# Performance work log

Hardware: AMD Instinct MI355X
Metric: run time of the kernel (lower is better)

Reference implementation:

```python
import jax, jax.numpy as jnp
import numpy as np

D_MODEL = 1024
NUM_HEADS = 16
D_K = D_MODEL // NUM_HEADS
THETA = 10000.0


def _rope(x, cos, sin):
    # x: [b, h, l, d_k]; cos/sin: [l, d_k//2]
    x1 = x[..., ::2]
    x2 = x[..., 1::2]
    re = x1 * cos - x2 * sin
    ro = x1 * sin + x2 * cos
    return jnp.stack([re, ro], axis=-1).reshape(x.shape)


def setup_inputs() -> dict:
    key = jax.random.key(0)
    k0, k1, k2, k3, k4 = jax.random.split(key, 5)
    b, l = 2, 2048
    scale = 1.0 / np.sqrt(D_MODEL)
    return {
        "in_features": jax.random.normal(k0, (b, l, D_MODEL), dtype=jnp.float32),
        "wq": jax.random.normal(k1, (D_MODEL, D_MODEL), dtype=jnp.float32) * scale,
        "wk": jax.random.normal(k2, (D_MODEL, D_MODEL), dtype=jnp.float32) * scale,
        "wv": jax.random.normal(k3, (D_MODEL, D_MODEL), dtype=jnp.float32) * scale,
        "wo": jax.random.normal(k4, (D_MODEL, D_MODEL), dtype=jnp.float32) * scale,
    }


def reference(in_features, wq, wk, wv, wo):
    b, l, d = in_features.shape
    h, dk = NUM_HEADS, D_K

    def proj(w):
        # torch: einsum('b l d, k d -> b l k') == x @ w.T
        y = jnp.einsum('bld,kd->blk', in_features, w)
        return y.reshape(b, l, h, dk).transpose(0, 2, 1, 3)  # [b,h,l,dk]

    Q, K, V = proj(wq), proj(wk), proj(wv)

    # RoPE (use_rope=True)
    inv_freq = 1.0 / (THETA ** (jnp.arange(0, dk, 2, dtype=jnp.float32) / dk))
    angles = jnp.arange(l, dtype=jnp.float32)[:, None] * inv_freq[None, :]  # [l, dk//2]
    cos, sin = jnp.cos(angles), jnp.sin(angles)
    Q = _rope(Q, cos, sin)
    K = _rope(K, cos, sin)

    scores = jnp.einsum('bhqd,bhkd->bhqk', Q, K) / jnp.sqrt(jnp.float32(dk))
    causal = jnp.tril(jnp.ones((l, l), dtype=bool))  # [l,l]
    scores = jnp.where(causal[None, None], scores, jnp.float32(-jnp.inf))
    attn = jax.nn.softmax(scores, axis=-1)
    ctx = jnp.einsum('bhqk,bhkd->bhqd', attn, V)
    ctx = ctx.transpose(0, 2, 1, 3).reshape(b, l, d)  # [b,l,d_model]
    out = jnp.einsum('bld,md->blm', ctx, wo)
    return out
```

## Files before the change

kernel.cpp:

```cpp
#include <hip/hip_runtime.h>
#include <stdint.h>

typedef __attribute__((ext_vector_type(8))) short short8;
typedef __attribute__((ext_vector_type(4))) float floatx4;
typedef __attribute__((ext_vector_type(16))) float floatx16;

#define DEV static __device__ __forceinline__

DEV unsigned short f2bf(float f) {
  union { float f; uint32_t u; } v; v.f = f;
  return (unsigned short)((v.u + 0x7FFFu + ((v.u >> 16) & 1u)) >> 16);
}
DEV float bf2f(unsigned short h) {
  union { uint32_t u; float f; } v; v.u = ((uint32_t)h) << 16;
  return v.f;
}
DEV uint32_t cvtpk(float lo, float hi) {
  uint32_t d;
  asm("v_cvt_pk_bf16_f32 %0, %1, %2" : "=v"(d) : "v"(lo), "v"(hi));
  return d;
}
DEV void gload_lds16(const void* g, void* l) {
  __builtin_amdgcn_global_load_lds(
      (const __attribute__((address_space(1))) uint32_t*)g,
      (__attribute__((address_space(3))) uint32_t*)l, 16, 0, 0);
}

#if defined(__has_builtin)
#if __has_builtin(__builtin_amdgcn_permlane32_swap)
#define HAVE_PLSWAP 1
#endif
#endif
DEV void plswap(uint32_t& a, uint32_t& b) {
#ifdef HAVE_PLSWAP
  typedef unsigned int u2v __attribute__((ext_vector_type(2)));
  u2v r = __builtin_amdgcn_permlane32_swap(a, b, false, false);
  a = r.x; b = r.y;
#else
  uint32_t sa = (uint32_t)__shfl_xor((int)a, 32);
  uint32_t sb = (uint32_t)__shfl_xor((int)b, 32);
  uint32_t lane = __lane_id();
  uint32_t na = lane < 32 ? a : sb;
  uint32_t nb = lane < 32 ? sa : b;
  a = na; b = nb;
#endif
}
DEV float xmax32(float x) {
  union { float f; uint32_t u; } a, b; a.f = x; b.f = x;
  plswap(a.u, b.u);
  return fmaxf(a.f, b.f);
}
DEV float xsum32(float x) {
  union { float f; uint32_t u; } a, b; a.f = x; b.f = x;
  plswap(a.u, b.u);
  return a.f + b.f;
}

__global__ __launch_bounds__(256) void k_convert(
    const float* __restrict__ X, const float* __restrict__ Wq,
    const float* __restrict__ Wk, const float* __restrict__ Wv,
    const float* __restrict__ Wo, unsigned short* __restrict__ out) {
  long gid = (long)blockIdx.x * 256 + threadIdx.x;
  long e = gid * 8;
  int seg = (int)(e >> 20);
  const float* src; long base;
  if (seg < 4)      { src = X;  base = 0; }
  else if (seg == 4){ src = Wq; base = 4l << 20; }
  else if (seg == 5){ src = Wk; base = 5l << 20; }
  else if (seg == 6){ src = Wv; base = 6l << 20; }
  else              { src = Wo; base = 7l << 20; }
  const float4* s4 = (const float4*)(src + (e - base));
  float4 a = s4[0], b = s4[1];
  union { uint4 q; unsigned short s[8]; } u;
  u.s[0] = f2bf(a.x); u.s[1] = f2bf(a.y); u.s[2] = f2bf(a.z); u.s[3] = f2bf(a.w);
  u.s[4] = f2bf(b.x); u.s[5] = f2bf(b.y); u.s[6] = f2bf(b.z); u.s[7] = f2bf(b.w);
  *(uint4*)(out + e) = u.q;
}

template <int MODE>
__global__ __launch_bounds__(256) void k_gemm(
    const unsigned short* __restrict__ A,
    const unsigned short* __restrict__ B0, const unsigned short* __restrict__ B1,
    const unsigned short* __restrict__ B2,
    unsigned short* __restrict__ Qo, unsigned short* __restrict__ Ko,
    unsigned short* __restrict__ VFo, float* __restrict__ Cf, int K) {
  __shared__ unsigned short At[128 * 64];
  __shared__ unsigned short Bt[128 * 64];
  const int tid = threadIdx.x, lane = tid & 63, wid = tid >> 6;
  const int wm = (wid >> 1) * 64, wn = (wid & 1) * 64;
  const int g = lane >> 4, c0 = lane & 15;
  const int bm0 = blockIdx.x * 128;
  const int bnG = blockIdx.y * 128;
  const unsigned short* Bp;
  int bn0;
  if constexpr (MODE == 0) {
    int wsel = bnG >> 10;
    Bp = wsel == 0 ? B0 : (wsel == 1 ? B1 : B2);
    bn0 = bnG & 1023;
  } else { Bp = B0; bn0 = bnG; }
  floatx4 acc[4][4] = {};
  const int nk = K >> 6;
  const int koff = (blockIdx.x + blockIdx.y * 3) & (nk - 1);
  const int swzr = (c0 & 7) << 4;
  for (int s = 0; s < nk; ++s) {
    const int kt = ((s + koff) & (nk - 1)) << 6;
#pragma unroll
    for (int i = 0; i < 4; ++i) {
      int o = (wid * 64 + lane) * 16 + i * 4096;
      int row = o >> 7;
      int col = (o & 127) ^ ((row & 7) << 4);
      int k0 = col >> 1;
      gload_lds16((const char*)A  + ((long)(bm0 + row) * K + kt + k0) * 2, (char*)At + o);
      gload_lds16((const char*)Bp + ((long)(bn0 + row) * K + kt + k0) * 2, (char*)Bt + o);
    }
    __syncthreads();
#pragma unroll
    for (int kk = 0; kk < 2; ++kk) {
      const int kb = kk * 64 + g * 16;
      short8 av[4], bv[4];
#pragma unroll
      for (int mi = 0; mi < 4; ++mi)
        av[mi] = *(const short8*)((const char*)At + (wm + mi * 16 + c0) * 128 + (kb ^ swzr));
#pragma unroll
      for (int ni = 0; ni < 4; ++ni)
        bv[ni] = *(const short8*)((const char*)Bt + (wn + ni * 16 + c0) * 128 + (kb ^ swzr));
#pragma unroll
      for (int mi = 0; mi < 4; ++mi)
#pragma unroll
        for (int ni = 0; ni < 4; ++ni)
          acc[mi][ni] = __builtin_amdgcn_mfma_f32_16x16x32_bf16(av[mi], bv[ni], acc[mi][ni], 0, 0, 0);
    }
    __syncthreads();
  }
  if constexpr (MODE == 1) {
#pragma unroll
    for (int mi = 0; mi < 4; ++mi)
#pragma unroll
      for (int ni = 0; ni < 4; ++ni)
#pragma unroll
        for (int i = 0; i < 4; ++i) {
          int r = bm0 + wm + mi * 16 + 4 * g + i;
          int cg = bnG + wn + ni * 16 + c0;
          Cf[(long)r * 1024 + cg] = acc[mi][ni][i];
        }
  } else {
    const int wsel = bnG >> 10;
#pragma unroll
    for (int mi = 0; mi < 4; ++mi)
#pragma unroll
      for (int ni = 0; ni < 4; ++ni)
#pragma unroll
        for (int i = 0; i < 4; ++i) {
          int r = bm0 + wm + mi * 16 + 4 * g + i;
          int cg = bnG + wn + ni * 16 + c0;
          int cc = cg & 1023, head = cc >> 6, dkk = cc & 63;
          int bb = r >> 11, ll = r & 2047;
          long bh = bb * 16 + head;
          float v = acc[mi][ni][i];
          if (wsel == 2) {
            int T = ll >> 6, rt = ll & 63;
            int m = rt >> 4, hb = (rt >> 3) & 1, j = rt & 7;
            int dvs = dkk >> 5, c = dkk & 31;
            VFo[bh * 131072 + T * 4096 + (dvs * 4 + m) * 512 + (hb * 32 + c) * 8 + j] = f2bf(v);
          } else {
            unsigned short* dst = wsel == 0 ? Qo : Ko;
            dst[(bh * 2048 + ll) * 64 + dkk] = f2bf(v);
          }
        }
  }
}

__global__ __launch_bounds__(256) void k_rope(unsigned short* __restrict__ Qd, float qscale) {
  int gid = blockIdx.x * 256 + threadIdx.x;
  int row = gid >> 1, hf = gid & 1;
  int l = row & 2047;
  unsigned short* p = Qd + (long)row * 64 + hf * 32;
  union { uint4 q[4]; unsigned short s[32]; } u;
#pragma unroll
  for (int i = 0; i < 4; ++i) u.q[i] = ((const uint4*)p)[i];
  float lf = (float)l;
#pragma unroll
  for (int j = 0; j < 16; ++j) {
    int pp = hf * 16 + j;
    float ang = lf * exp2f(-(float)pp * 0.4152410118609203f);
    float sv, cv; sincosf(ang, &sv, &cv);
    float x1 = bf2f(u.s[2 * j]), x2 = bf2f(u.s[2 * j + 1]);
    u.s[2 * j]     = f2bf((x1 * cv - x2 * sv) * qscale);
    u.s[2 * j + 1] = f2bf((x1 * sv + x2 * cv) * qscale);
  }
#pragma unroll
  for (int i = 0; i < 4; ++i) ((uint4*)p)[i] = u.q[i];
}

__global__ __launch_bounds__(256) void k_ropeK_repack(
    const unsigned short* __restrict__ Kin, unsigned short* __restrict__ KF) {
  const int blk = blockIdx.x;
  const int bh = blk >> 5, T = blk & 31;
  const int tid = threadIdx.x;
  const unsigned short* src = Kin + ((long)bh * 2048 + T * 64) * 64;
  unsigned short* dst = KF + (long)blk * 4096;
#pragma unroll
  for (int it = 0; it < 2; ++it) {
    int u = tid + it * 256;
    int lane = u & 63, kd = u >> 6;
    int kvs = kd >> 2, dseg = kd & 3;
    int row = kvs * 32 + (lane & 31);
    int col = dseg * 16 + 8 * (lane >> 5);
    union { uint4 q; unsigned short s[8]; } v;
    v.q = *(const uint4*)(src + row * 64 + col);
    float lf = (float)(T * 64 + row);
#pragma unroll
    for (int j = 0; j < 4; ++j) {
      int p = (col >> 1) + j;
      float ang = lf * exp2f(-(float)p * 0.4152410118609203f);
      float sv, cv; sincosf(ang, &sv, &cv);
      float x1 = bf2f(v.s[2 * j]), x2 = bf2f(v.s[2 * j + 1]);
      v.s[2 * j]     = f2bf(x1 * cv - x2 * sv);
      v.s[2 * j + 1] = f2bf(x1 * sv + x2 * cv);
    }
    *(uint4*)(dst + u * 8) = v.q;
  }
}

DEV void attn_tile(int T, int Tend, int ntm1, int qabs, int h, int c,
                   const unsigned short* __restrict__ kfbase,
                   const unsigned short* __restrict__ vfbase,
                   const short8 (&qf)[4],
                   const short8 (&kc0)[4], const short8 (&kc1)[4],
                   short8 (&kn0)[4], short8 (&kn1)[4],
                   floatx16& ctx0, floatx16& ctx1, float& m_, float& l_) {
  {
    const int Tn = T + 1 < Tend ? T + 1 : T;
    const unsigned short* kt = kfbase + (long)Tn * 4096;
#pragma unroll
    for (int d = 0; d < 4; ++d) kn0[d] = *(const short8*)(kt + d * 512);
#pragma unroll
    for (int d = 0; d < 4; ++d) kn1[d] = *(const short8*)(kt + 2048 + d * 512);
  }
  const unsigned short* vt = vfbase + (long)T * 4096;
  short8 vf0[4], vf1[4];
#pragma unroll
  for (int m = 0; m < 4; ++m) vf0[m] = *(const short8*)(vt + m * 512);
#pragma unroll
  for (int m = 0; m < 4; ++m) vf1[m] = *(const short8*)(vt + 2048 + m * 512);

  floatx16 s0 = {}, s1 = {};
#pragma unroll
  for (int d = 0; d < 4; ++d)
    s0 = __builtin_amdgcn_mfma_f32_32x32x16_bf16(kc0[d], qf[d], s0, 0, 0, 0);
#pragma unroll
  for (int d = 0; d < 4; ++d)
    s1 = __builtin_amdgcn_mfma_f32_32x32x16_bf16(kc1[d], qf[d], s1, 0, 0, 0);

  if (T == ntm1) {
    const int kvb = T * 64 + 4 * h;
#pragma unroll
    for (int r = 0; r < 16; ++r) {
      const int off = (r & 3) + 8 * (r >> 2);
      if (kvb + off > qabs) s0[r] = -1e30f;
      if (kvb + 32 + off > qabs) s1[r] = -1e30f;
    }
  }
  float a4[8];
#pragma unroll
  for (int j = 0; j < 4; ++j) {
    a4[j]     = fmaxf(fmaxf(s0[4 * j], s0[4 * j + 1]), fmaxf(s0[4 * j + 2], s0[4 * j + 3]));
    a4[4 + j] = fmaxf(fmaxf(s1[4 * j], s1[4 * j + 1]), fmaxf(s1[4 * j + 2], s1[4 * j + 3]));
  }
  float mx = fmaxf(fmaxf(fmaxf(a4[0], a4[1]), fmaxf(a4[2], a4[3])),
                   fmaxf(fmaxf(a4[4], a4[5]), fmaxf(a4[6], a4[7])));
  mx = xmax32(mx);
  if (!__all(mx <= m_ + 8.0f)) {
    float mn = fmaxf(m_, mx);
    float sc = exp2f(m_ - mn);
    m_ = mn;
    l_ *= sc;
#pragma unroll
    for (int r = 0; r < 16; ++r) { ctx0[r] *= sc; ctx1[r] *= sc; }
  }
#pragma unroll
  for (int r = 0; r < 16; ++r) s0[r] = exp2f(s0[r] - m_);
#pragma unroll
  for (int r = 0; r < 16; ++r) s1[r] = exp2f(s1[r] - m_);
  float b4[8];
#pragma unroll
  for (int j = 0; j < 4; ++j) {
    b4[j]     = (s0[4 * j] + s0[4 * j + 1]) + (s0[4 * j + 2] + s0[4 * j + 3]);
    b4[4 + j] = (s1[4 * j] + s1[4 * j + 1]) + (s1[4 * j + 2] + s1[4 * j + 3]);
  }
  float rs = ((b4[0] + b4[1]) + (b4[2] + b4[3])) + ((b4[4] + b4[5]) + (b4[6] + b4[7]));
  rs = xsum32(rs);
  l_ += rs;

  uint32_t pd0[8], pd1[8];
#pragma unroll
  for (int d = 0; d < 8; ++d) {
    pd0[d] = cvtpk(s0[2 * d], s0[2 * d + 1]);
    pd1[d] = cvtpk(s1[2 * d], s1[2 * d + 1]);
  }
#pragma unroll
  for (int kvs = 0; kvs < 2; ++kvs) {
    const uint32_t* pd = kvs ? pd1 : pd0;
#pragma unroll
    for (int ks = 0; ks < 2; ++ks) {
      uint32_t u0 = pd[4 * ks], u2 = pd[4 * ks + 2];
      uint32_t u1 = pd[4 * ks + 1], u3 = pd[4 * ks + 3];
      plswap(u0, u2);
      plswap(u1, u3);
      union { uint32_t u[4]; short8 s; } bu;
      bu.u[0] = u0; bu.u[1] = u1; bu.u[2] = u2; bu.u[3] = u3;
      ctx0 = __builtin_amdgcn_mfma_f32_32x32x16_bf16(vf0[kvs * 2 + ks], bu.s, ctx0, 0, 0, 0);
      ctx1 = __builtin_amdgcn_mfma_f32_32x32x16_bf16(vf1[kvs * 2 + ks], bu.s, ctx1, 0, 0, 0);
    }
  }
}

__global__ __launch_bounds__(128) void k_attn(
    const unsigned short* __restrict__ Q, const unsigned short* __restrict__ KF,
    const unsigned short* __restrict__ VF, unsigned short* __restrict__ O) {
  __shared__ float lctx[64][33];
  __shared__ float lml[64][2];
  const int bid = blockIdx.x;
  const int xcd = bid & 7, idx = bid >> 3;
  const int head = idx >> 6;
  const int a = idx & 63;
  const int qs = (head < 2) ? a : 63 - a;
  const int bh = xcd * 4 + head;
  const int tid = threadIdx.x;
  const int wid = tid >> 6, lane = tid & 63;
  const int h = lane >> 5, c = lane & 31;
  const unsigned short* Qh = Q + (long)bh * 2048 * 64;
  const unsigned short* kfbase = KF + (long)bh * 131072 + lane * 8;
  const unsigned short* vfbase = VF + (long)bh * 131072 + lane * 8;
  const int q0 = qs * 32, qabs = q0 + c;
  const int nt = (qs >> 1) + 1, ntm1 = nt - 1;
  const int h0 = nt >> 1;
  const int Tbeg = wid ? h0 : 0;
  const int Tend = wid ? nt : h0;

  short8 qf[4];
#pragma unroll
  for (int d = 0; d < 4; ++d)
    qf[d] = *(const short8*)(Qh + (long)(q0 + c) * 64 + d * 16 + 8 * h);

  floatx16 ctx0 = {}, ctx1 = {};
  float m_ = -1e30f, l_ = 0.f;

  if (Tbeg < Tend) {
    short8 kA0[4], kA1[4], kB0[4], kB1[4];
    const unsigned short* kt0 = kfbase + (long)Tbeg * 4096;
#pragma unroll
    for (int d = 0; d < 4; ++d) kA0[d] = *(const short8*)(kt0 + d * 512);
#pragma unroll
    for (int d = 0; d < 4; ++d) kA1[d] = *(const short8*)(kt0 + 2048 + d * 512);
    int T = Tbeg;
    while (true) {
      attn_tile(T, Tend, ntm1, qabs, h, c, kfbase, vfbase, qf, kA0, kA1, kB0, kB1, ctx0, ctx1, m_, l_);
      if (++T >= Tend) break;
      attn_tile(T, Tend, ntm1, qabs, h, c, kfbase, vfbase, qf, kB0, kB1, kA0, kA1, ctx0, ctx1, m_, l_);
      if (++T >= Tend) break;
    }
  }
  if (wid) {
#pragma unroll
    for (int r = 0; r < 16; ++r) {
      lctx[lane][r] = ctx0[r];
      lctx[lane][16 + r] = ctx1[r];
    }
    lml[lane][0] = m_;
    lml[lane][1] = l_;
  }
  __syncthreads();
  if (!wid) {
    float m1 = lml[lane][0], l1 = lml[lane][1];
    float m = fmaxf(m_, m1);
    float e0 = exp2f(m_ - m), e1 = exp2f(m1 - m);
    float inv = 1.f / (l_ * e0 + l1 * e1);
    const int b = bh >> 4, hd = bh & 15;
    unsigned short* orow = O + (long)(b * 2048 + q0 + c) * 1024 + hd * 64;
#pragma unroll
    for (int m4 = 0; m4 < 4; ++m4) {
      uint2 w0, w1;
      w0.x = cvtpk((ctx0[4 * m4]     * e0 + lctx[lane][4 * m4]     * e1) * inv,
                   (ctx0[4 * m4 + 1] * e0 + lctx[lane][4 * m4 + 1] * e1) * inv);
      w0.y = cvtpk((ctx0[4 * m4 + 2] * e0 + lctx[lane][4 * m4 + 2] * e1) * inv,
                   (ctx0[4 * m4 + 3] * e0 + lctx[lane][4 * m4 + 3] * e1) * inv);
      *(uint2*)(orow + 8 * m4 + 4 * h) = w0;
      w1.x = cvtpk((ctx1[4 * m4]     * e0 + lctx[lane][16 + 4 * m4]     * e1) * inv,
                   (ctx1[4 * m4 + 1] * e0 + lctx[lane][16 + 4 * m4 + 1] * e1) * inv);
      w1.y = cvtpk((ctx1[4 * m4 + 2] * e0 + lctx[lane][16 + 4 * m4 + 2] * e1) * inv,
                   (ctx1[4 * m4 + 3] * e0 + lctx[lane][16 + 4 * m4 + 3] * e1) * inv);
      *(uint2*)(orow + 32 + 8 * m4 + 4 * h) = w1;
    }
  }
}

extern "C" void kernel_launch(void* const* d_in, const int* in_sizes, int n_in,
                              void* d_out, int out_size, void* d_ws, size_t ws_size,
                              hipStream_t stream) {
  const float* X  = (const float*)d_in[0];
  const float* Wq = (const float*)d_in[1];
  const float* Wk = (const float*)d_in[2];
  const float* Wv = (const float*)d_in[3];
  const float* Wo = (const float*)d_in[4];
  unsigned short* Xb  = (unsigned short*)d_ws;
  unsigned short* Wqb = Xb + (4l << 20);
  unsigned short* Wkb = Xb + (5l << 20);
  unsigned short* Wvb = Xb + (6l << 20);
  unsigned short* Wob = Xb + (7l << 20);
  unsigned short* Qw  = Xb + (8l << 20);
  unsigned short* Kw  = Xb + (12l << 20);
  unsigned short* VFw = Xb + (16l << 20);
  unsigned short* KFw = Xb;
  unsigned short* Cw  = Xb + (20l << 20);
  float* Out = (float*)d_out;

  k_convert<<<4096, 256, 0, stream>>>(X, Wq, Wk, Wv, Wo, Xb);
  k_gemm<0><<<dim3(32, 24), 256, 0, stream>>>(Xb, Wqb, Wkb, Wvb, Qw, Kw, VFw, nullptr, 1024);
  k_rope<<<512, 256, 0, stream>>>(Qw, 0.18033688011112042f);
  k_ropeK_repack<<<1024, 256, 0, stream>>>(Kw, KFw);
  k_attn<<<2048, 128, 0, stream>>>(Qw, KFw, VFw, Cw);
  k_gemm<1><<<dim3(32, 8), 256, 0, stream>>>(Cw, Wob, nullptr, nullptr,
                                             nullptr, nullptr, nullptr, Out, 1024);
}
```

Baseline: 134.1 us.

## Split attention KV range across four waves and merge Q/K RoPE kernels

```diff
diff --git a/kernel.cpp b/kernel.cpp
--- a/kernel.cpp
+++ b/kernel.cpp
@@ -170,55 +170,57 @@
   }
 }
 
-__global__ __launch_bounds__(256) void k_rope(unsigned short* __restrict__ Qd, float qscale) {
-  int gid = blockIdx.x * 256 + threadIdx.x;
-  int row = gid >> 1, hf = gid & 1;
-  int l = row & 2047;
-  unsigned short* p = Qd + (long)row * 64 + hf * 32;
-  union { uint4 q[4]; unsigned short s[32]; } u;
-#pragma unroll
-  for (int i = 0; i < 4; ++i) u.q[i] = ((const uint4*)p)[i];
-  float lf = (float)l;
-#pragma unroll
-  for (int j = 0; j < 16; ++j) {
-    int pp = hf * 16 + j;
-    float ang = lf * exp2f(-(float)pp * 0.4152410118609203f);
-    float sv, cv; sincosf(ang, &sv, &cv);
-    float x1 = bf2f(u.s[2 * j]), x2 = bf2f(u.s[2 * j + 1]);
-    u.s[2 * j]     = f2bf((x1 * cv - x2 * sv) * qscale);
-    u.s[2 * j + 1] = f2bf((x1 * sv + x2 * cv) * qscale);
-  }
-#pragma unroll
-  for (int i = 0; i < 4; ++i) ((uint4*)p)[i] = u.q[i];
-}
-
-__global__ __launch_bounds__(256) void k_ropeK_repack(
-    const unsigned short* __restrict__ Kin, unsigned short* __restrict__ KF) {
+__global__ __launch_bounds__(256) void k_ropeQK(
+    unsigned short* __restrict__ Qd, const unsigned short* __restrict__ Kin,
+    unsigned short* __restrict__ KF, float qscale) {
   const int blk = blockIdx.x;
-  const int bh = blk >> 5, T = blk & 31;
   const int tid = threadIdx.x;
-  const unsigned short* src = Kin + ((long)bh * 2048 + T * 64) * 64;
-  unsigned short* dst = KF + (long)blk * 4096;
-#pragma unroll
-  for (int it = 0; it < 2; ++it) {
-    int u = tid + it * 256;
-    int lane = u & 63, kd = u >> 6;
-    int kvs = kd >> 2, dseg = kd & 3;
-    int row = kvs * 32 + (lane & 31);
-    int col = dseg * 16 + 8 * (lane >> 5);
-    union { uint4 q; unsigned short s[8]; } v;
-    v.q = *(const uint4*)(src + row * 64 + col);
-    float lf = (float)(T * 64 + row);
-#pragma unroll
-    for (int j = 0; j < 4; ++j) {
-      int p = (col >> 1) + j;
-      float ang = lf * exp2f(-(float)p * 0.4152410118609203f);
+  if (blk < 512) {
+    int gid = blk * 256 + tid;
+    int row = gid >> 1, hf = gid & 1;
+    int l = row & 2047;
+    unsigned short* p = Qd + (long)row * 64 + hf * 32;
+    union { uint4 q[4]; unsigned short s[32]; } u;
+#pragma unroll
+    for (int i = 0; i < 4; ++i) u.q[i] = ((const uint4*)p)[i];
+    float lf = (float)l;
+#pragma unroll
+    for (int j = 0; j < 16; ++j) {
+      int pp = hf * 16 + j;
+      float ang = lf * exp2f(-(float)pp * 0.4152410118609203f);
       float sv, cv; sincosf(ang, &sv, &cv);
-      float x1 = bf2f(v.s[2 * j]), x2 = bf2f(v.s[2 * j + 1]);
-      v.s[2 * j]     = f2bf(x1 * cv - x2 * sv);
-      v.s[2 * j + 1] = f2bf(x1 * sv + x2 * cv);
-    }
-    *(uint4*)(dst + u * 8) = v.q;
+      float x1 = bf2f(u.s[2 * j]), x2 = bf2f(u.s[2 * j + 1]);
+      u.s[2 * j]     = f2bf((x1 * cv - x2 * sv) * qscale);
+      u.s[2 * j + 1] = f2bf((x1 * sv + x2 * cv) * qscale);
+    }
+#pragma unroll
+    for (int i = 0; i < 4; ++i) ((uint4*)p)[i] = u.q[i];
+  } else {
+    const int kblk = blk - 512;
+    const int bh = kblk >> 5, T = kblk & 31;
+    const unsigned short* src = Kin + ((long)bh * 2048 + T * 64) * 64;
+    unsigned short* dst = KF + (long)kblk * 4096;
+#pragma unroll
+    for (int it = 0; it < 2; ++it) {
+      int u = tid + it * 256;
+      int lane = u & 63, kd = u >> 6;
+      int kvs = kd >> 2, dseg = kd & 3;
+      int row = kvs * 32 + (lane & 31);
+      int col = dseg * 16 + 8 * (lane >> 5);
+      union { uint4 q; unsigned short s[8]; } v;
+      v.q = *(const uint4*)(src + row * 64 + col);
+      float lf = (float)(T * 64 + row);
+#pragma unroll
+      for (int j = 0; j < 4; ++j) {
+        int p = (col >> 1) + j;
+        float ang = lf * exp2f(-(float)p * 0.4152410118609203f);
+        float sv, cv; sincosf(ang, &sv, &cv);
+        float x1 = bf2f(v.s[2 * j]), x2 = bf2f(v.s[2 * j + 1]);
+        v.s[2 * j]     = f2bf(x1 * cv - x2 * sv);
+        v.s[2 * j + 1] = f2bf(x1 * sv + x2 * cv);
+      }
+      *(uint4*)(dst + u * 8) = v.q;
+    }
   }
 }
 
@@ -315,16 +317,16 @@
   }
 }
 
-__global__ __launch_bounds__(128) void k_attn(
+__global__ __launch_bounds__(256) void k_attn(
     const unsigned short* __restrict__ Q, const unsigned short* __restrict__ KF,
     const unsigned short* __restrict__ VF, unsigned short* __restrict__ O) {
-  __shared__ float lctx[64][33];
-  __shared__ float lml[64][2];
+  __shared__ float lctx[3][64][33];
+  __shared__ float lml[3][64][2];
   const int bid = blockIdx.x;
   const int xcd = bid & 7, idx = bid >> 3;
   const int head = idx >> 6;
   const int a = idx & 63;
-  const int qs = (head < 2) ? a : 63 - a;
+  const int qs = 63 - a;
   const int bh = xcd * 4 + head;
   const int tid = threadIdx.x;
   const int wid = tid >> 6, lane = tid & 63;
@@ -334,9 +336,8 @@
   const unsigned short* vfbase = VF + (long)bh * 131072 + lane * 8;
   const int q0 = qs * 32, qabs = q0 + c;
   const int nt = (qs >> 1) + 1, ntm1 = nt - 1;
-  const int h0 = nt >> 1;
-  const int Tbeg = wid ? h0 : 0;
-  const int Tend = wid ? nt : h0;
+  const int Tbeg = (nt * wid) >> 2;
+  const int Tend = (nt * (wid + 1)) >> 2;
 
   short8 qf[4];
 #pragma unroll
@@ -364,33 +365,48 @@
   if (wid) {
 #pragma unroll
     for (int r = 0; r < 16; ++r) {
-      lctx[lane][r] = ctx0[r];
-      lctx[lane][16 + r] = ctx1[r];
-    }
-    lml[lane][0] = m_;
-    lml[lane][1] = l_;
+      lctx[wid - 1][lane][r] = ctx0[r];
+      lctx[wid - 1][lane][16 + r] = ctx1[r];
+    }
+    lml[wid - 1][lane][0] = m_;
+    lml[wid - 1][lane][1] = l_;
   }
   __syncthreads();
   if (!wid) {
-    float m1 = lml[lane][0], l1 = lml[lane][1];
-    float m = fmaxf(m_, m1);
-    float e0 = exp2f(m_ - m), e1 = exp2f(m1 - m);
-    float inv = 1.f / (l_ * e0 + l1 * e1);
+    float m = m_;
+#pragma unroll
+    for (int p = 0; p < 3; ++p) m = fmaxf(m, lml[p][lane][0]);
+    float e0 = exp2f(m_ - m);
+    float ep[3];
+    float lsum = l_ * e0;
+#pragma unroll
+    for (int p = 0; p < 3; ++p) {
+      ep[p] = exp2f(lml[p][lane][0] - m);
+      lsum += lml[p][lane][1] * ep[p];
+    }
+    float inv = 1.f / lsum;
     const int b = bh >> 4, hd = bh & 15;
     unsigned short* orow = O + (long)(b * 2048 + q0 + c) * 1024 + hd * 64;
 #pragma unroll
-    for (int m4 = 0; m4 < 4; ++m4) {
-      uint2 w0, w1;
-      w0.x = cvtpk((ctx0[4 * m4]     * e0 + lctx[lane][4 * m4]     * e1) * inv,
-                   (ctx0[4 * m4 + 1] * e0 + lctx[lane][4 * m4 + 1] * e1) * inv);
-      w0.y = cvtpk((ctx0[4 * m4 + 2] * e0 + lctx[lane][4 * m4 + 2] * e1) * inv,
-                   (ctx0[4 * m4 + 3] * e0 + lctx[lane][4 * m4 + 3] * e1) * inv);
-      *(uint2*)(orow + 8 * m4 + 4 * h) = w0;
-      w1.x = cvtpk((ctx1[4 * m4]     * e0 + lctx[lane][16 + 4 * m4]     * e1) * inv,
-                   (ctx1[4 * m4 + 1] * e0 + lctx[lane][16 + 4 * m4 + 1] * e1) * inv);
-      w1.y = cvtpk((ctx1[4 * m4 + 2] * e0 + lctx[lane][16 + 4 * m4 + 2] * e1) * inv,
-                   (ctx1[4 * m4 + 3] * e0 + lctx[lane][16 + 4 * m4 + 3] * e1) * inv);
-      *(uint2*)(orow + 32 + 8 * m4 + 4 * h) = w1;
+    for (int m4 = 0; m4 < 8; ++m4) {
+      const bool hi = m4 >= 4;
+      const int r0 = (m4 & 3) * 4;
+      float v0 = (hi ? ctx1[r0]     : ctx0[r0])     * e0;
+      float v1 = (hi ? ctx1[r0 + 1] : ctx0[r0 + 1]) * e0;
+      float v2 = (hi ? ctx1[r0 + 2] : ctx0[r0 + 2]) * e0;
+      float v3 = (hi ? ctx1[r0 + 3] : ctx0[r0 + 3]) * e0;
+      const int lr = (hi ? 16 : 0) + r0;
+#pragma unroll
+      for (int p = 0; p < 3; ++p) {
+        v0 += lctx[p][lane][lr]     * ep[p];
+        v1 += lctx[p][lane][lr + 1] * ep[p];
+        v2 += lctx[p][lane][lr + 2] * ep[p];
+        v3 += lctx[p][lane][lr + 3] * ep[p];
+      }
+      uint2 w;
+      w.x = cvtpk(v0 * inv, v1 * inv);
+      w.y = cvtpk(v2 * inv, v3 * inv);
+      *(uint2*)(orow + (hi ? 32 : 0) + 8 * (m4 & 3) + 4 * h) = w;
     }
   }
 }
@@ -417,9 +433,8 @@
 
   k_convert<<<4096, 256, 0, stream>>>(X, Wq, Wk, Wv, Wo, Xb);
   k_gemm<0><<<dim3(32, 24), 256, 0, stream>>>(Xb, Wqb, Wkb, Wvb, Qw, Kw, VFw, nullptr, 1024);
-  k_rope<<<512, 256, 0, stream>>>(Qw, 0.18033688011112042f);
-  k_ropeK_repack<<<1024, 256, 0, stream>>>(Kw, KFw);
-  k_attn<<<2048, 128, 0, stream>>>(Qw, KFw, VFw, Cw);
+  k_ropeQK<<<1536, 256, 0, stream>>>(Qw, Kw, KFw, 0.18033688011112042f);
+  k_attn<<<2048, 256, 0, stream>>>(Qw, KFw, VFw, Cw);
   k_gemm<1><<<dim3(32, 8), 256, 0, stream>>>(Cw, Wob, nullptr, nullptr,
                                              nullptr, nullptr, nullptr, Out, 1024);
 }
```

New measurement: 132.8 us. No clear change (-0.9%).
